# Kernel tuning notes

Measured on AMD Instinct MI355X. Metric: run time of the kernel, lower is better.

Reference implementation:

```python
import jax, jax.numpy as jnp
import numpy as np

N_SLOTS = 32


def entmax15(z):
    """Exact 1.5-entmax along last axis (Peters et al. 2019 closed form)."""
    x = z / 2.0
    x = x - jnp.max(x, axis=-1, keepdims=True)
    zs = jnp.flip(jnp.sort(x, axis=-1), axis=-1)  # descending
    n = zs.shape[-1]
    k = jnp.arange(1, n + 1, dtype=zs.dtype)
    mean = jnp.cumsum(zs, axis=-1) / k
    meansq = jnp.cumsum(zs * zs, axis=-1) / k
    ss = k * (meansq - mean * mean)
    delta = (1.0 - ss) / k
    tau = mean - jnp.sqrt(jnp.maximum(delta, 0.0))
    support = jnp.sum(tau <= zs, axis=-1) - 1  # index of last valid k
    tau_star = jnp.take_along_axis(tau, support[..., None], axis=-1)
    p = jnp.maximum(x - tau_star, 0.0)
    return p * p


def dual_memory_scan(x_seq, W_h, W_x, b_h, W_write, n_slots):
    """E25 entmax dual-memory recurrence. x_seq: [B,T,D]."""
    B, T, D = x_seq.shape
    scale = 1.0 / jnp.sqrt(jnp.array(D, dtype=x_seq.dtype))
    tape0 = jnp.zeros((B, n_slots, D), dtype=x_seq.dtype)
    work0 = jnp.zeros((B, D), dtype=x_seq.dtype)
    # precompute input projection for all timesteps
    xw = jnp.einsum('btd,ed->bte', x_seq, W_x)  # [B,T,D]

    def step(carry, x_t):
        tape, work = carry
        h_pre = work @ W_h.T + x_t + b_h                    # [B,D]
        # entmax read over tape slots
        r_scores = jnp.einsum('bnd,bd->bn', tape, h_pre) * scale
        a = entmax15(r_scores)                              # [B,n]
        read = jnp.einsum('bn,bnd->bd', a, tape)
        h_new = jnp.tanh(h_pre + read)                      # [B,D]
        # entmax write back to tape
        w_val = h_new @ W_write.T                           # [B,D]
        w_scores = jnp.einsum('bnd,bd->bn', tape, h_new) * scale
        b = entmax15(w_scores)                              # [B,n]
        tape_new = tape + b[..., None] * (w_val[:, None, :] - tape)
        return (tape_new, h_new), h_new

    (tape_f, work_f), hs = jax.lax.scan(step, (tape0, work0), jnp.swapaxes(xw, 0, 1))
    out = jnp.swapaxes(hs, 0, 1)  # [B,T,D]
    return out, tape_f, work_f


def setup_inputs() -> dict:
    key = jax.random.key(0)
    ks = jax.random.split(key, 7)
    B, T, D = 8, 1024, 512
    s = 0.02
    return {
        'x': jax.random.normal(ks[0], (B, T, D), dtype=jnp.float32),
        'W_in': jax.random.normal(ks[1], (2 * D, D), dtype=jnp.float32) * s,
        'W_out': jax.random.normal(ks[2], (D, D), dtype=jnp.float32) * s,
        'W_h': jax.random.normal(ks[3], (D, D), dtype=jnp.float32) * s,
        'W_x': jax.random.normal(ks[4], (D, D), dtype=jnp.float32) * s,
        'b_h': jnp.zeros((D,), dtype=jnp.float32),
        'W_write': jax.random.normal(ks[5], (D, D), dtype=jnp.float32) * s,
    }


def reference(x, W_in, W_out, W_h, W_x, b_h, W_write):
    d_inner = W_out.shape[1]
    xz = x @ W_in.T                                   # [B,T,2*d_inner]
    x_proj, z = xz[..., :d_inner], xz[..., d_inner:]
    x_proj = jax.nn.silu(x_proj)
    out, tape_f, work_f = dual_memory_scan(x_proj, W_h, W_x, b_h, W_write, N_SLOTS)
    out = out * jax.nn.silu(z)
    out = out @ W_out.T
    return out, tape_f, work_f
```

## Files before the change

kernel.cpp:

```cpp
#include <hip/hip_runtime.h>


#define BB 8
#define TT 1024
#define DD 512
#define NS 32
#define KW 8

static constexpr float SCALE = 0.044194173824159216f;

__device__ __forceinline__ float siluf(float v) { return v / (1.0f + __expf(-v)); }

template <int CTRL>
__device__ __forceinline__ float dpp_add(float x) {
  int xi = __builtin_bit_cast(int, x);
  int yi = __builtin_amdgcn_update_dpp(0, xi, CTRL, 0xF, 0xF, false);
  return x + __builtin_bit_cast(float, yi);
}
template <int PAT>
__device__ __forceinline__ float swz_add(float x) {
  int yi = __builtin_amdgcn_ds_swizzle(__builtin_bit_cast(int, x), PAT);
  return x + __builtin_bit_cast(float, yi);
}
__device__ __forceinline__ float reduce8(float x) {
  x = swz_add<0x041F>(x);
  x = swz_add<0x081F>(x);
  x = swz_add<0x101F>(x);
  return x;
}
__device__ __forceinline__ float reduce32(float x) {
  x = dpp_add<0x121>(x);
  x = dpp_add<0x122>(x);
  x = dpp_add<0x124>(x);
  x = dpp_add<0x128>(x);
  return swz_add<0x401F>(x);
}

__device__ __forceinline__ float entmax32(float z, int l32) {
  float x = 0.5f * z;
  float m = x;
  #pragma unroll
  for (int d = 1; d < 32; d <<= 1) m = fmaxf(m, __shfl_xor(m, d, 32));
  x -= m;
  float s = x;
  #pragma unroll
  for (int k = 2; k <= 32; k <<= 1) {
    #pragma unroll
    for (int j = k >> 1; j > 0; j >>= 1) {
      float y    = __shfl_xor(s, j, 32);
      bool lower = (l32 & j) == 0;
      bool desc  = (l32 & k) == 0;
      s = (desc ^ lower) ? fminf(s, y) : fmaxf(s, y);
    }
  }
  float cs = s, cq = s * s;
  #pragma unroll
  for (int d = 1; d < 32; d <<= 1) {
    float ts = __shfl_up(cs, d, 32);
    float tq = __shfl_up(cq, d, 32);
    if (l32 >= d) { cs += ts; cq += tq; }
  }
  float kf    = (float)(l32 + 1);
  float mean  = cs / kf;
  float msq   = cq / kf;
  float ssv   = kf * (msq - mean * mean);
  float delta = (1.0f - ssv) / kf;
  float tau   = mean - sqrtf(fmaxf(delta, 0.0f));
  unsigned long long mask = __ballot(tau <= s);
  int support = __popcll(mask & 0xFFFFFFFFull) - 1;
  float tau_star = __shfl(tau, support, 32);
  float p = fmaxf(x - tau_star, 0.0f);
  return p * p;
}

template <int MODE>
__global__ __launch_bounds__(256) void gemm_tn(const float* __restrict__ A,
                                               const float* __restrict__ Bm,
                                               float* __restrict__ C0,
                                               float* __restrict__ C1,
                                               int M, int N, int K) {
  const int bm = blockIdx.x, bn = blockIdx.y;
  const int tid = threadIdx.x;
  const int tx = tid & 15, ty = tid >> 4;
  __shared__ __align__(16) float As[16][132];
  __shared__ __align__(16) float Bs[16][132];
  float acc[8][8] = {};
  const int rowA0 = bm * 128, rowB0 = bn * 128;

  for (int k0 = 0; k0 < K; k0 += 16) {
    #pragma unroll
    for (int q = 0; q < 2; ++q) {
      int idx = tid + q * 256;
      int r   = idx >> 2;
      int kq  = (idx & 3) * 4;
      float4 a4 = *(const float4*)&A [(size_t)(rowA0 + r) * K + k0 + kq];
      float4 b4 = *(const float4*)&Bm[(size_t)(rowB0 + r) * K + k0 + kq];
      As[kq + 0][r] = a4.x; As[kq + 1][r] = a4.y; As[kq + 2][r] = a4.z; As[kq + 3][r] = a4.w;
      Bs[kq + 0][r] = b4.x; Bs[kq + 1][r] = b4.y; Bs[kq + 2][r] = b4.z; Bs[kq + 3][r] = b4.w;
    }
    __syncthreads();
    #pragma unroll
    for (int kk = 0; kk < 16; ++kk) {
      float4 a0 = *(const float4*)&As[kk][ty * 8];
      float4 a1 = *(const float4*)&As[kk][ty * 8 + 4];
      float4 b0 = *(const float4*)&Bs[kk][tx * 8];
      float4 b1 = *(const float4*)&Bs[kk][tx * 8 + 4];
      float av[8] = {a0.x, a0.y, a0.z, a0.w, a1.x, a1.y, a1.z, a1.w};
      float bv[8] = {b0.x, b0.y, b0.z, b0.w, b1.x, b1.y, b1.z, b1.w};
      #pragma unroll
      for (int i = 0; i < 8; ++i)
        #pragma unroll
        for (int j = 0; j < 8; ++j) acc[i][j] = fmaf(av[i], bv[j], acc[i][j]);
    }
    __syncthreads();
  }
  #pragma unroll
  for (int i = 0; i < 8; ++i) {
    int gr = rowA0 + ty * 8 + i;
    #pragma unroll
    for (int j = 0; j < 8; ++j) {
      int gc = rowB0 + tx * 8 + j;
      float v = acc[i][j];
      if (MODE == 0) {
        float sv = siluf(v);
        if (gc < 512) C0[(size_t)gr * 512 + gc]         = sv;
        else          C1[(size_t)gr * 512 + (gc - 512)] = sv;
      } else {
        C0[(size_t)gr * N + gc] = v;
      }
    }
  }
}

__global__ __launch_bounds__(1024) void scan_kernel(
    const float* __restrict__ Wh, const float* __restrict__ Ww,
    const float* __restrict__ bh, const float* __restrict__ XW,
    const float* __restrict__ SZ, float* __restrict__ Y,
    unsigned long long* __restrict__ Pp,
    float* __restrict__ outTape, float* __restrict__ outWork) {
  const int tid  = threadIdx.x;
  const int wv   = tid >> 6, lane = tid & 63;
  const int b    = blockIdx.x & 7, g = blockIdx.x >> 3;
  const int l32  = lane & 31;
  const int seg  = lane & 7;
  const int row  = tid >> 3;
  const int frow = g * 128 + row;

  __shared__ float tape[NS][DD];
  __shared__ float h_full[DD], hp[DD], wvv[DD], bhs[DD];
  __shared__ float ws_arr[NS], q1_arr[NS], q2s;
  __shared__ float bArr[NS], aArr[NS];

  float w[64];
  {
    const float* src = (frow < DD) ? (Wh + (size_t)frow * DD)
                                   : (Ww + (size_t)(frow - DD) * DD);
    #pragma unroll
    for (int q = 0; q < 16; ++q) {
      int c4 = seg * 64 + ((4 * q + 4 * seg) & 63);
      float4 v4 = *(const float4*)(src + c4);
      w[4*q+0] = v4.x; w[4*q+1] = v4.y; w[4*q+2] = v4.z; w[4*q+3] = v4.w;
    }
  }
  for (int e = tid; e < NS * DD; e += 1024) ((float*)tape)[e] = 0.f;
  if (tid < DD) { h_full[tid] = 0.f; bhs[tid] = bh[tid]; }
  __syncthreads();

  for (int t = 0; t <= TT; ++t) {
    unsigned long long* pbuf = Pp + ((size_t)(t & 1) * BB + b) * 1024;
    float pv = 0.f;
    #pragma unroll
    for (int q = 0; q < 16; ++q) {
      int c4 = seg * 64 + ((4 * q + 4 * seg) & 63);
      float4 h4 = *(const float4*)&h_full[c4];
      pv = fmaf(w[4*q+0], h4.x, pv);
      pv = fmaf(w[4*q+1], h4.y, pv);
      pv = fmaf(w[4*q+2], h4.z, pv);
      pv = fmaf(w[4*q+3], h4.w, pv);
    }
    pv = reduce8(pv);
    if (seg == 0) {
      unsigned long long u =
          ((unsigned long long)(unsigned)(t + 1) << 32) |
          (unsigned long long)__builtin_bit_cast(unsigned, pv);
      __hip_atomic_store(&pbuf[frow], u, __ATOMIC_RELAXED, __HIP_MEMORY_SCOPE_AGENT);
    }
    float x_in = 0.f, szv = 0.f;
    if (t < TT && tid < DD) {
      x_in = XW[((size_t)b * TT + t) * DD + tid];
      if ((tid >> 6) == g) szv = SZ[((size_t)b * TT + t) * DD + tid];
    }
    {
      int n = wv * 2 + (lane >> 5);
      float sw = 0.f;
      #pragma unroll
      for (int j = 0; j < 16; ++j)
        sw = fmaf(tape[n][l32 + 32 * j], h_full[l32 + 32 * j], sw);
      sw = reduce32(sw);
      if (l32 == 0) ws_arr[n] = sw * SCALE;
    }
    __syncthreads();
    if (wv == 1) {
      float pb = entmax32(ws_arr[l32], l32);
      if (lane < NS) bArr[lane] = pb;
    }
    {
      const unsigned want = (unsigned)(t + 1);
      unsigned long long u;
      do {
        u = __hip_atomic_load(&pbuf[tid], __ATOMIC_RELAXED, __HIP_MEMORY_SCOPE_AGENT);
      } while ((unsigned)(u >> 32) != want);
      float s = __builtin_bit_cast(float, (unsigned)(u & 0xFFFFFFFFu));
      if (tid < DD) hp[tid] = s + x_in + bhs[tid];
      else          wvv[tid - DD] = s;
    }
    __syncthreads();
    if (t < TT) {
      int n = wv * 2 + (lane >> 5);
      float s1 = 0.f;
      #pragma unroll
      for (int j = 0; j < 16; ++j)
        s1 = fmaf(tape[n][l32 + 32 * j], hp[l32 + 32 * j], s1);
      s1 = reduce32(s1);
      if (l32 == 0) q1_arr[n] = s1;
      if (wv == 0) {
        float s2 = 0.f;
        #pragma unroll
        for (int j = 0; j < 8; ++j)
          s2 = fmaf(wvv[lane + 64 * j], hp[lane + 64 * j], s2);
        s2 = reduce32(s2);
        s2 += __shfl_xor(s2, 32, 64);
        if (lane == 0) q2s = s2;
      }
    }
    __syncthreads();
    if (wv == 0) {
      if (t < TT) {
        float pb = bArr[l32];
        float rs = SCALE * fmaf(pb, q2s - q1_arr[l32], q1_arr[l32]);
        float pa = entmax32(rs, l32);
        if (lane < NS) aArr[lane] = pa;
      }
    } else {
      for (int e = tid - 64; e < NS * DD; e += 960) {
        int n = e >> 9, d = e & 511;
        float tv = tape[n][d];
        tape[n][d] = fmaf(bArr[n], wvv[d] - tv, tv);
      }
    }
    __syncthreads();
    if (t == TT) {
      if (tid < DD && (tid >> 6) == g) outWork[(size_t)b * DD + tid] = h_full[tid];
      for (int e = tid; e < NS * 64; e += 1024) {
        int n = e >> 6, d = g * 64 + (e & 63);
        outTape[((size_t)b * NS + n) * DD + d] = tape[n][d];
      }
      break;
    }
    if (tid < DD) {
      float r = 0.f;
      #pragma unroll
      for (int n = 0; n < NS; ++n) r = fmaf(aArr[n], tape[n][tid], r);
      float hn = tanhf(hp[tid] + r);
      if ((tid >> 6) == g)
        Y[((size_t)b * TT + t) * DD + tid] = hn * szv;
      h_full[tid] = hn;
    }
    __syncthreads();
  }
}

extern "C" void kernel_launch(void* const* d_in, const int* in_sizes, int n_in,
                              void* d_out, int out_size, void* d_ws, size_t ws_size,
                              hipStream_t stream) {
  (void)in_sizes; (void)n_in; (void)out_size; (void)ws_size;
  const float* x    = (const float*)d_in[0];
  const float* W_in = (const float*)d_in[1];
  const float* W_out= (const float*)d_in[2];
  const float* W_h  = (const float*)d_in[3];
  const float* W_x  = (const float*)d_in[4];
  const float* b_h  = (const float*)d_in[5];
  const float* W_wr = (const float*)d_in[6];

  float* out     = (float*)d_out;
  float* outTape = out + (size_t)BB * TT * DD;
  float* outWork = outTape + (size_t)BB * NS * DD;

  float* wsf  = (float*)d_ws;
  float* XP   = wsf;
  float* SZ   = XP + (size_t)BB * TT * DD;
  float* XWb  = SZ + (size_t)BB * TT * DD;
  unsigned long long* Pp = (unsigned long long*)(XWb + (size_t)BB * TT * DD);

  gemm_tn<0><<<dim3(64, 8), 256, 0, stream>>>(x, W_in, XP, SZ, BB * TT, 2 * DD, DD);
  gemm_tn<1><<<dim3(64, 4), 256, 0, stream>>>(XP, W_x, XWb, nullptr, BB * TT, DD, DD);
  scan_kernel<<<64, 1024, 0, stream>>>(W_h, W_wr, b_h, XWb, SZ, XP,
                                       Pp, outTape, outWork);
  gemm_tn<1><<<dim3(64, 4), 256, 0, stream>>>(XP, W_out, out, nullptr, BB * TT, DD, DD);
}
```

Before: 6.198 ms.

## Distribute read-score dot products across blocks and publish partials via flags

Each block now owns a 64-row slice of both the h_pre and write-value rows and adds the input and bias locally before publishing. It then computes partial tape·h_pre and w·h_pre dot products over its own 64-column slice and publishes them through extra flag slots. The post-exchange phase therefore only sums eight partials instead of recomputing full 512-wide dot products, which removes one block barrier per step. The change also replaces shuffle-based entmax reductions and sort steps with DPP/swizzle cross-lane ops and vectorises the tape update with float4. In exchange there are more flagged global stores and polls per step, plus an extra barrier before the partial computation.

```diff
diff --git a/kernel.cpp b/kernel.cpp
--- a/kernel.cpp
+++ b/kernel.cpp
@@ -6,6 +6,7 @@
 #define DD 512
 #define NS 32
 #define KW 8
+#define SLOTS 1288
 
 static constexpr float SCALE = 0.044194173824159216f;
 
@@ -21,6 +22,19 @@
 __device__ __forceinline__ float swz_add(float x) {
   int yi = __builtin_amdgcn_ds_swizzle(__builtin_bit_cast(int, x), PAT);
   return x + __builtin_bit_cast(float, yi);
+}
+template <int J>
+__device__ __forceinline__ float xlane(float x) {
+  if constexpr (J == 1) {
+    int yi = __builtin_amdgcn_update_dpp(0, __builtin_bit_cast(int, x), 0xB1, 0xF, 0xF, false);
+    return __builtin_bit_cast(float, yi);
+  } else if constexpr (J == 2) {
+    int yi = __builtin_amdgcn_update_dpp(0, __builtin_bit_cast(int, x), 0x4E, 0xF, 0xF, false);
+    return __builtin_bit_cast(float, yi);
+  } else {
+    int yi = __builtin_amdgcn_ds_swizzle(__builtin_bit_cast(int, x), (J << 10) | 0x1F);
+    return __builtin_bit_cast(float, yi);
+  }
 }
 __device__ __forceinline__ float reduce8(float x) {
   x = swz_add<0x041F>(x);
@@ -39,20 +53,18 @@
 __device__ __forceinline__ float entmax32(float z, int l32) {
   float x = 0.5f * z;
   float m = x;
-  #pragma unroll
-  for (int d = 1; d < 32; d <<= 1) m = fmaxf(m, __shfl_xor(m, d, 32));
+  m = fmaxf(m, xlane<1>(m));  m = fmaxf(m, xlane<2>(m));
+  m = fmaxf(m, xlane<4>(m));  m = fmaxf(m, xlane<8>(m));
+  m = fmaxf(m, xlane<16>(m));
   x -= m;
   float s = x;
-  #pragma unroll
-  for (int k = 2; k <= 32; k <<= 1) {
-    #pragma unroll
-    for (int j = k >> 1; j > 0; j >>= 1) {
-      float y    = __shfl_xor(s, j, 32);
-      bool lower = (l32 & j) == 0;
-      bool desc  = (l32 & k) == 0;
-      s = (desc ^ lower) ? fminf(s, y) : fmaxf(s, y);
-    }
-  }
+#define XST(K, J) { float y = xlane<J>(s); bool up = (((l32 & K) == 0) ^ ((l32 & J) == 0)); s = up ? fminf(s, y) : fmaxf(s, y); }
+  XST(2, 1)
+  XST(4, 2)  XST(4, 1)
+  XST(8, 4)  XST(8, 2)  XST(8, 1)
+  XST(16, 8) XST(16, 4) XST(16, 2) XST(16, 1)
+  XST(32, 16) XST(32, 8) XST(32, 4) XST(32, 2) XST(32, 1)
+#undef XST
   float cs = s, cq = s * s;
   #pragma unroll
   for (int d = 1; d < 32; d <<= 1) {
@@ -71,6 +83,20 @@
   float tau_star = __shfl(tau, support, 32);
   float p = fmaxf(x - tau_star, 0.0f);
   return p * p;
+}
+
+__device__ __forceinline__ void pubv(unsigned long long* p, int t, float v) {
+  unsigned long long u = ((unsigned long long)(unsigned)(t + 1) << 32) |
+                         (unsigned long long)__builtin_bit_cast(unsigned, v);
+  __hip_atomic_store(p, u, __ATOMIC_RELAXED, __HIP_MEMORY_SCOPE_AGENT);
+}
+__device__ __forceinline__ float pollv(const unsigned long long* p, int t) {
+  const unsigned want = (unsigned)(t + 1);
+  unsigned long long u;
+  do {
+    u = __hip_atomic_load(p, __ATOMIC_RELAXED, __HIP_MEMORY_SCOPE_AGENT);
+  } while ((unsigned)(u >> 32) != want);
+  return __builtin_bit_cast(float, (unsigned)(u & 0xFFFFFFFFu));
 }
 
 template <int MODE>
@@ -142,19 +168,19 @@
   const int wv   = tid >> 6, lane = tid & 63;
   const int b    = blockIdx.x & 7, g = blockIdx.x >> 3;
   const int l32  = lane & 31;
-  const int seg  = lane & 7;
+  const int seg  = tid & 7;
   const int row  = tid >> 3;
-  const int frow = g * 128 + row;
 
   __shared__ float tape[NS][DD];
-  __shared__ float h_full[DD], hp[DD], wvv[DD], bhs[DD];
-  __shared__ float ws_arr[NS], q1_arr[NS], q2s;
+  __shared__ float h_full[DD], hpC[DD], wvvC[DD];
+  __shared__ float hp_loc[64], wv_loc[64];
+  __shared__ float ws_arr[NS], q1part[KW * NS], q2part[KW];
   __shared__ float bArr[NS], aArr[NS];
 
   float w[64];
   {
-    const float* src = (frow < DD) ? (Wh + (size_t)frow * DD)
-                                   : (Ww + (size_t)(frow - DD) * DD);
+    const float* src = (row < 64) ? (Wh + (size_t)(g * 64 + row) * DD)
+                                  : (Ww + (size_t)(g * 64 + row - 64) * DD);
     #pragma unroll
     for (int q = 0; q < 16; ++q) {
       int c4 = seg * 64 + ((4 * q + 4 * seg) & 63);
@@ -162,12 +188,20 @@
       w[4*q+0] = v4.x; w[4*q+1] = v4.y; w[4*q+2] = v4.z; w[4*q+3] = v4.w;
     }
   }
+  const float bhv = (seg == 0 && row < 64) ? bh[g * 64 + row] : 0.f;
   for (int e = tid; e < NS * DD; e += 1024) ((float*)tape)[e] = 0.f;
-  if (tid < DD) { h_full[tid] = 0.f; bhs[tid] = bh[tid]; }
+  if (tid < DD) h_full[tid] = 0.f;
   __syncthreads();
 
   for (int t = 0; t <= TT; ++t) {
-    unsigned long long* pbuf = Pp + ((size_t)(t & 1) * BB + b) * 1024;
+    unsigned long long* pbuf = Pp + ((size_t)(t & 1) * BB + b) * SLOTS;
+    float xwv = 0.f;
+    if (seg == 0 && row < 64 && t < TT)
+      xwv = XW[((size_t)b * TT + t) * DD + g * 64 + row];
+    float szv = 0.f;
+    if (t < TT && tid < DD && (tid >> 6) == g)
+      szv = SZ[((size_t)b * TT + t) * DD + tid];
+
     float pv = 0.f;
     #pragma unroll
     for (int q = 0; q < 16; ++q) {
@@ -180,15 +214,24 @@
     }
     pv = reduce8(pv);
     if (seg == 0) {
-      unsigned long long u =
-          ((unsigned long long)(unsigned)(t + 1) << 32) |
-          (unsigned long long)__builtin_bit_cast(unsigned, pv);
-      __hip_atomic_store(&pbuf[frow], u, __ATOMIC_RELAXED, __HIP_MEMORY_SCOPE_AGENT);
-    }
-    float x_in = 0.f, szv = 0.f;
-    if (t < TT && tid < DD) {
-      x_in = XW[((size_t)b * TT + t) * DD + tid];
-      if ((tid >> 6) == g) szv = SZ[((size_t)b * TT + t) * DD + tid];
+      float hv = (row < 64) ? (pv + xwv + bhv) : pv;
+      if (row < 64) hp_loc[row] = hv; else wv_loc[row - 64] = hv;
+      pubv(&pbuf[g * 128 + row], t, hv);
+    }
+    __syncthreads();
+
+    {
+      int n = wv * 2 + (lane >> 5);
+      float s1 = fmaf(tape[n][g * 64 + 2 * l32],     hp_loc[2 * l32],
+               tape[n][g * 64 + 2 * l32 + 1] * hp_loc[2 * l32 + 1]);
+      s1 = reduce32(s1);
+      if (l32 == 0) pubv(&pbuf[1024 + g * 33 + n], t, s1);
+      if (wv == 0 && lane < 32) {
+        float s2 = fmaf(wv_loc[l32], hp_loc[l32],
+                        wv_loc[l32 + 32] * hp_loc[l32 + 32]);
+        s2 = reduce32(s2);
+        if (l32 == 0) pubv(&pbuf[1024 + g * 33 + 32], t, s2);
+      }
     }
     {
       int n = wv * 2 + (lane >> 5);
@@ -200,55 +243,53 @@
       if (l32 == 0) ws_arr[n] = sw * SCALE;
     }
     __syncthreads();
+
     if (wv == 1) {
       float pb = entmax32(ws_arr[l32], l32);
       if (lane < NS) bArr[lane] = pb;
     }
     {
-      const unsigned want = (unsigned)(t + 1);
-      unsigned long long u;
-      do {
-        u = __hip_atomic_load(&pbuf[tid], __ATOMIC_RELAXED, __HIP_MEMORY_SCOPE_AGENT);
-      } while ((unsigned)(u >> 32) != want);
-      float s = __builtin_bit_cast(float, (unsigned)(u & 0xFFFFFFFFu));
-      if (tid < DD) hp[tid] = s + x_in + bhs[tid];
-      else          wvv[tid - DD] = s;
-    }
-    __syncthreads();
-    if (t < TT) {
-      int n = wv * 2 + (lane >> 5);
-      float s1 = 0.f;
-      #pragma unroll
-      for (int j = 0; j < 16; ++j)
-        s1 = fmaf(tape[n][l32 + 32 * j], hp[l32 + 32 * j], s1);
-      s1 = reduce32(s1);
-      if (l32 == 0) q1_arr[n] = s1;
-      if (wv == 0) {
-        float s2 = 0.f;
-        #pragma unroll
-        for (int j = 0; j < 8; ++j)
-          s2 = fmaf(wvv[lane + 64 * j], hp[lane + 64 * j], s2);
-        s2 = reduce32(s2);
-        s2 += __shfl_xor(s2, 32, 64);
-        if (lane == 0) q2s = s2;
-      }
-    }
-    __syncthreads();
+      float v = pollv(&pbuf[tid], t);
+      int i = tid & 127, gg = tid >> 7;
+      if (i < 64) hpC[gg * 64 + i] = v;
+      else        wvvC[gg * 64 + (i - 64)] = v;
+      if (tid < KW * 33) {
+        float v2 = pollv(&pbuf[1024 + tid], t);
+        int gg2 = tid / 33, j2 = tid - gg2 * 33;
+        if (j2 < 32) q1part[gg2 * 32 + j2] = v2;
+        else         q2part[gg2] = v2;
+      }
+    }
+    __syncthreads();
+
     if (wv == 0) {
       if (t < TT) {
+        float q1s = 0.f, q2s = 0.f;
+        #pragma unroll
+        for (int k = 0; k < KW; ++k) {
+          q1s += q1part[k * 32 + l32];
+          q2s += q2part[k];
+        }
         float pb = bArr[l32];
-        float rs = SCALE * fmaf(pb, q2s - q1_arr[l32], q1_arr[l32]);
+        float rs = SCALE * fmaf(pb, q2s - q1s, q1s);
         float pa = entmax32(rs, l32);
         if (lane < NS) aArr[lane] = pa;
       }
     } else {
-      for (int e = tid - 64; e < NS * DD; e += 960) {
-        int n = e >> 9, d = e & 511;
-        float tv = tape[n][d];
-        tape[n][d] = fmaf(bArr[n], wvv[d] - tv, tv);
-      }
-    }
-    __syncthreads();
+      for (int e = tid - 64; e < NS * DD / 4; e += 960) {
+        int n = e >> 7, dq = (e & 127) * 4;
+        float  bn = bArr[n];
+        float4 tv = *(float4*)&tape[n][dq];
+        float4 wq = *(const float4*)&wvvC[dq];
+        tv.x = fmaf(bn, wq.x - tv.x, tv.x);
+        tv.y = fmaf(bn, wq.y - tv.y, tv.y);
+        tv.z = fmaf(bn, wq.z - tv.z, tv.z);
+        tv.w = fmaf(bn, wq.w - tv.w, tv.w);
+        *(float4*)&tape[n][dq] = tv;
+      }
+    }
+    __syncthreads();
+
     if (t == TT) {
       if (tid < DD && (tid >> 6) == g) outWork[(size_t)b * DD + tid] = h_full[tid];
       for (int e = tid; e < NS * 64; e += 1024) {
@@ -261,7 +302,7 @@
       float r = 0.f;
       #pragma unroll
       for (int n = 0; n < NS; ++n) r = fmaf(aArr[n], tape[n][tid], r);
-      float hn = tanhf(hp[tid] + r);
+      float hn = tanhf(hpC[tid] + r);
       if ((tid >> 6) == g)
         Y[((size_t)b * TT + t) * DD + tid] = hn * szv;
       h_full[tid] = hn;
```

Measured after the change: 5.453 ms. 12.0% less time.
